# Optimization experiments

Hardware: AMD Instinct MI355X
Metric: run time of the kernel (lower is better)

The kernel has to match this reference:

```python
import jax, jax.numpy as jnp
import numpy as np

B, T, C, H, HS = 4, 2048, 1024, 16, 64
EPS = 1e-5


def setup_inputs() -> dict:
    key = jax.random.key(0)
    ks = jax.random.split(key, 16)
    s = lambda k, shp, fan: jax.random.normal(k, shp, jnp.float32) * (fan ** -0.5)
    return {
        "x": jax.random.normal(ks[0], (B, T, C), jnp.float32),
        "wq": s(ks[1], (H, C, HS), C), "bq": jnp.zeros((H, HS), jnp.float32),
        "wk": s(ks[2], (H, C, HS), C), "bk": jnp.zeros((H, HS), jnp.float32),
        "wv": s(ks[3], (H, C, HS), C), "bv": jnp.zeros((H, HS), jnp.float32),
        "wp": s(ks[4], (C, C), C), "bp": jnp.zeros((C,), jnp.float32),
        "w1": s(ks[5], (C, 4 * C), C), "b1": jnp.zeros((4 * C,), jnp.float32),
        "w2": s(ks[6], (4 * C, C), 4 * C), "b2": jnp.zeros((C,), jnp.float32),
        "g1": jnp.ones((C,), jnp.float32), "be1": jnp.zeros((C,), jnp.float32),
        "g2": jnp.ones((C,), jnp.float32), "be2": jnp.zeros((C,), jnp.float32),
    }


def _layernorm(x, g, b):
    mu = jnp.mean(x, axis=-1, keepdims=True)
    var = jnp.mean(jnp.square(x - mu), axis=-1, keepdims=True)
    return (x - mu) * jax.lax.rsqrt(var + EPS) * g + b


def reference(x, wq, bq, wk, bk, wv, bv, wp, bp, w1, b1, w2, b2, g1, be1, g2, be2):
    Bc, Tc, Cc = x.shape
    h = _layernorm(x, g1, be1)
    # per-head projections stacked: [B,H,T,HS]
    q = jnp.einsum('btc,hcd->bhtd', h, wq) + bq[None, :, None, :]
    k = jnp.einsum('btc,hcd->bhtd', h, wk) + bk[None, :, None, :]
    v = jnp.einsum('btc,hcd->bhtd', h, wv) + bv[None, :, None, :]
    # NOTE: source scales by 1/sqrt(n_embd), not 1/sqrt(head_size)
    scores = jnp.einsum('bhtd,bhsd->bhts', q, k) * (Cc ** -0.5)
    causal = jnp.tril(jnp.ones((Tc, Tc), bool))
    scores = jnp.where(causal, scores, -jnp.inf)
    attn = jax.nn.softmax(scores, axis=-1)
    out = jnp.einsum('bhts,bhsd->bhtd', attn, v)
    out = out.transpose(0, 2, 1, 3).reshape(Bc, Tc, Cc)  # concat heads
    x = x + out @ wp + bp
    h2 = _layernorm(x, g2, be2)
    ffn = jax.nn.relu(h2 @ w1 + b1) @ w2 + b2
    return x + ffn
```

## Files before the change

kernel.cpp:

```cpp
#include <hip/hip_runtime.h>


constexpr int Bb = 4, Tt = 2048, Cc = 1024, Hh = 16, HSz = 64, Ff = 4096;
constexpr int Mrows = Bb * Tt;

typedef __attribute__((ext_vector_type(8))) short bf16x8;
typedef __attribute__((ext_vector_type(4))) float f32x4;

__device__ __forceinline__ ushort f2bf(float f) {
  uint u = __builtin_bit_cast(uint, f);
  uint r = (u + 0x7fffu + ((u >> 16) & 1u)) >> 16;
  return (ushort)r;
}
__device__ __forceinline__ float bf2f(ushort s) {
  return __builtin_bit_cast(float, ((uint)s) << 16);
}
__device__ __forceinline__ uint cvtpk_bf16(float lo, float hi) {
  uint r;
  asm("v_cvt_pk_bf16_f32 %0, %1, %2" : "=v"(r) : "v"(lo), "v"(hi));
  return r;
}
__device__ __forceinline__ void gload16(const void* g, void* l) {
  __builtin_amdgcn_global_load_lds(
      (const __attribute__((address_space(1))) void*)g,
      (__attribute__((address_space(3))) void*)l, 16, 0, 0);
}
#define VMCNT(n) asm volatile("s_waitcnt vmcnt(" #n ")" ::: "memory")
#define LGKM0                                          \
  do {                                                 \
    asm volatile("s_waitcnt lgkmcnt(0)" ::: "memory"); \
    __builtin_amdgcn_sched_barrier(0);                 \
  } while (0)
#define BARRIER __builtin_amdgcn_s_barrier()

__device__ __forceinline__ void ln_body(const float* __restrict__ x,
                                        const float* __restrict__ g,
                                        const float* __restrict__ b,
                                        ushort* __restrict__ out, int row) {
  const float* xr = x + (size_t)row * Cc;
  int c4 = threadIdx.x * 4;
  float4 v = *(const float4*)(xr + c4);
  float s1 = v.x + v.y + v.z + v.w;
  float s2 = v.x * v.x + v.y * v.y + v.z * v.z + v.w * v.w;
#pragma unroll
  for (int off = 32; off >= 1; off >>= 1) {
    s1 += __shfl_xor(s1, off);
    s2 += __shfl_xor(s2, off);
  }
  __shared__ float red[8];
  int wid = threadIdx.x >> 6, lane = threadIdx.x & 63;
  if (lane == 0) { red[wid] = s1; red[4 + wid] = s2; }
  __syncthreads();
  float t1 = red[0] + red[1] + red[2] + red[3];
  float t2 = red[4] + red[5] + red[6] + red[7];
  float mu = t1 * (1.0f / Cc);
  float var = t2 * (1.0f / Cc) - mu * mu;
  float rs = rsqrtf(var + 1e-5f);
  float4 gv = *(const float4*)(g + c4);
  float4 bv = *(const float4*)(b + c4);
  ushort4 o;
  o.x = f2bf((v.x - mu) * rs * gv.x + bv.x);
  o.y = f2bf((v.y - mu) * rs * gv.y + bv.y);
  o.z = f2bf((v.z - mu) * rs * gv.z + bv.z);
  o.w = f2bf((v.w - mu) * rs * gv.w + bv.w);
  *(ushort4*)(out + (size_t)row * Cc + c4) = o;
}

__global__ __launch_bounds__(256) void ln_kernel(const float* __restrict__ x,
                                                 const float* __restrict__ g,
                                                 const float* __restrict__ b,
                                                 ushort* __restrict__ out) {
  ln_body(x, g, b, out, blockIdx.x);
}

__device__ __forceinline__ void tcast_body(const float* __restrict__ src,
                                           ushort* __restrict__ dst, int ldS,
                                           int ldD, int r0, int c0) {
  __shared__ float t[32][33];
  int c = threadIdx.x & 31, r8 = threadIdx.x >> 5;
#pragma unroll
  for (int i = 0; i < 4; ++i) {
    int r = r8 + i * 8;
    t[r][c] = src[(size_t)(r0 + r) * ldS + c0 + c];
  }
  __syncthreads();
#pragma unroll
  for (int i = 0; i < 4; ++i) {
    int rr = r8 + i * 8;
    dst[(size_t)(c0 + rr) * ldD + r0 + c] = f2bf(t[c][rr]);
  }
}

__global__ __launch_bounds__(256) void prep_kernel(
    const float* __restrict__ wq, const float* __restrict__ wk,
    const float* __restrict__ wv, const float* __restrict__ wp,
    const float* __restrict__ w1, const float* __restrict__ w2,
    const float* __restrict__ bq, const float* __restrict__ bk,
    const float* __restrict__ bv, ushort* __restrict__ wqkvT,
    ushort* __restrict__ wpT, ushort* __restrict__ w1T,
    ushort* __restrict__ w2T, float* __restrict__ bqkv,
    const float* __restrict__ x, const float* __restrict__ g1,
    const float* __restrict__ be1, ushort* __restrict__ h1b) {
  int id = blockIdx.x;
  if (id < 3072) {
    int z = id >> 6, rem = id & 63;
    int zz = z >> 4, h = z & 15;
    const float* src =
        (zz == 0 ? wq : (zz == 1 ? wk : wv)) + (size_t)h * Cc * HSz;
    ushort* d = wqkvT + (size_t)(zz * 1024 + h * 64) * 1024;
    tcast_body(src, d, HSz, Cc, (rem & 31) * 32, (rem >> 5) * 32);
  } else if (id < 4096) {
    int rem = id - 3072;
    tcast_body(wp, wpT, 1024, 1024, (rem & 31) * 32, (rem >> 5) * 32);
  } else if (id < 8192) {
    int rem = id - 4096;
    tcast_body(w1, w1T, 4096, 1024, (rem & 31) * 32, (rem >> 5) * 32);
  } else if (id < 12288) {
    int rem = id - 8192;
    tcast_body(w2, w2T, 1024, 4096, (rem & 127) * 32, (rem >> 7) * 32);
  } else if (id < 12300) {
    int i = (id - 12288) * 256 + threadIdx.x;
    bqkv[i] = i < 1024 ? bq[i] : (i < 2048 ? bk[i - 1024] : bv[i - 2048]);
  } else {
    ln_body(x, g1, be1, h1b, id - 12300);
  }
}

__device__ __forceinline__ void xcd_swz(int& bx, int& by) {
  int bid = blockIdx.x + blockIdx.y * gridDim.x;
  int cpx = (gridDim.x * gridDim.y) >> 3;
  int id = (bid & 7) * cpx + (bid >> 3);
  bx = id % gridDim.x;
  by = id / gridDim.x;
}

template <int MH, int NH>
__device__ __forceinline__ void mfma16(f32x4 (&acc)[8][4], bf16x8 (&a)[4][2],
                                       bf16x8 (&b)[2][2]) {
#pragma unroll
  for (int m = 0; m < 4; ++m)
#pragma unroll
    for (int n = 0; n < 2; ++n)
#pragma unroll
      for (int kk = 0; kk < 2; ++kk)
        acc[MH * 4 + m][NH * 2 + n] = __builtin_amdgcn_mfma_f32_16x16x32_bf16(
            a[m][kk], b[n][kk], acc[MH * 4 + m][NH * 2 + n], 0, 0, 0);
}

__device__ __forceinline__ void gemm256_main(const ushort* __restrict__ A,
                                             const ushort* __restrict__ Bt,
                                             int m0, int n0,
                                             ushort* __restrict__ As,
                                             ushort* __restrict__ Bs,
                                             f32x4 (&acc)[8][4]) {
  constexpr int NKT = 16;
  int tid = threadIdx.x, wid = tid >> 6, lane = tid & 63;
  int wr = wid >> 2, wc = wid & 3, fr = lane & 15, fq = lane >> 4;
  const ushort* Ag = A + (size_t)m0 * 1024;
  const ushort* Bg = Bt + (size_t)n0 * 1024;
  int r0 = tid >> 3, r1 = 64 + (tid >> 3);
  int sc = ((tid & 7) ^ ((tid >> 3) & 7)) << 3;

  auto stage = [&](int ktn, int h, int ns) {
    const ushort* g = (h < 2) ? Ag : Bg;
    ushort* l = ((h < 2) ? As : Bs) + ns * 16384 + (h & 1) * 8192;
    int kcol = ktn * 64, rbase = (h & 1) * 128;
    gload16(g + (size_t)(rbase + r0) * 1024 + kcol + sc, l + (size_t)wid * 512);
    gload16(g + (size_t)(rbase + r1) * 1024 + kcol + sc,
            l + (size_t)(512 + wid * 64) * 8);
  };
  auto readA = [&](int slot, int mh, bf16x8 (&a)[4][2]) {
#pragma unroll
    for (int m = 0; m < 4; ++m) {
      int row = wr * 128 + mh * 64 + m * 16 + fr;
#pragma unroll
      for (int kk = 0; kk < 2; ++kk)
        a[m][kk] = *(const bf16x8*)&As[slot * 16384 + row * 64 +
                                       (((kk * 4 + fq) ^ (row & 7)) << 3)];
    }
  };
  auto readB = [&](int slot, int nh, bf16x8 (&b)[2][2]) {
#pragma unroll
    for (int n = 0; n < 2; ++n) {
      int row = wc * 64 + nh * 32 + n * 16 + fr;
#pragma unroll
      for (int kk = 0; kk < 2; ++kk)
        b[n][kk] = *(const bf16x8*)&Bs[slot * 16384 + row * 64 +
                                       (((kk * 4 + fq) ^ (row & 7)) << 3)];
    }
  };

  stage(0, 0, 0); stage(0, 1, 0); stage(0, 2, 0); stage(0, 3, 0);
  VMCNT(0);
  BARRIER;

  bf16x8 a[4][2], b0[2][2], b1[2][2];
#pragma unroll 1
  for (int kt = 0; kt < NKT; ++kt) {
    int slot = kt & 1, ns = slot ^ 1;
    bool st = (kt + 1 < NKT);
    readA(slot, 0, a);
    readB(slot, 0, b0);
    if (st) { stage(kt + 1, 0, ns); stage(kt + 1, 2, ns); }
    BARRIER;
    LGKM0;
    __builtin_amdgcn_s_setprio(1);
    mfma16<0, 0>(acc, a, b0);
    __builtin_amdgcn_s_setprio(0);
    BARRIER;
    readB(slot, 1, b1);
    if (st) { stage(kt + 1, 1, ns); stage(kt + 1, 3, ns); }
    BARRIER;
    LGKM0;
    __builtin_amdgcn_s_setprio(1);
    mfma16<0, 1>(acc, a, b1);
    __builtin_amdgcn_s_setprio(0);
    BARRIER;
    readA(slot, 1, a);
    BARRIER;
    LGKM0;
    __builtin_amdgcn_s_setprio(1);
    mfma16<1, 0>(acc, a, b0);
    __builtin_amdgcn_s_setprio(0);
    BARRIER;
    __builtin_amdgcn_s_setprio(1);
    mfma16<1, 1>(acc, a, b1);
    __builtin_amdgcn_s_setprio(0);
    VMCNT(0);
    BARRIER;
  }
}

__global__ __launch_bounds__(512, 2) void gemm256_relu(
    const ushort* __restrict__ A, const ushort* __restrict__ Bt,
    const float* __restrict__ bias, ushort* __restrict__ Cout, int ldc) {
  __shared__ __align__(16) ushort As[2 * 256 * 64];
  __shared__ __align__(16) ushort Bs[2 * 256 * 64];
  f32x4 acc[8][4] = {};
  int bx, by;
  xcd_swz(bx, by);
  int m0 = by * 256, n0 = bx * 256;
  gemm256_main(A, Bt, m0, n0, As, Bs, acc);
  int lane = threadIdx.x & 63, wid = threadIdx.x >> 6;
  int wr = wid >> 2, wc = wid & 3, fr = lane & 15, fq = lane >> 4;
#pragma unroll
  for (int i = 0; i < 8; ++i) {
    int gm = m0 + wr * 128 + (i >> 2) * 64 + (i & 3) * 16 + fq * 4;
#pragma unroll
    for (int j2 = 0; j2 < 4; ++j2) {
      int gn = n0 + wc * 64 + (j2 >> 1) * 32 + (j2 & 1) * 16 + fr;
      float bsv = bias[gn];
#pragma unroll
      for (int j = 0; j < 4; ++j)
        Cout[(size_t)(gm + j) * ldc + gn] = f2bf(fmaxf(acc[i][j2][j] + bsv, 0.f));
    }
  }
}

__global__ __launch_bounds__(512, 2) void gemm192_qkv(
    const ushort* __restrict__ A, const ushort* __restrict__ Bt,
    const float* __restrict__ bias, ushort* __restrict__ q,
    ushort* __restrict__ k, ushort* __restrict__ vt) {
  __shared__ __align__(16) ushort As[2 * 256 * 64];
  __shared__ __align__(16) ushort Bs[2 * 192 * 64];
  f32x4 acc[8][3] = {};
  int bx, by;
  xcd_swz(bx, by);
  int m0 = by * 256, n0 = bx * 192;
  int tid = threadIdx.x, wid = tid >> 6, lane = tid & 63;
  int wr = wid >> 2, wc = wid & 3, fr = lane & 15, fq = lane >> 4;
  const ushort* Ag = A + (size_t)m0 * 1024;
  const ushort* Bg = Bt + (size_t)n0 * 1024;
  int r0 = tid >> 3;
  int sc = ((tid & 7) ^ ((tid >> 3) & 7)) << 3;
  constexpr int NKT = 16;

  auto stageA = [&](int ktn, int c, int ns) {
    ushort* l = As + ns * 16384 + c * 4096;
    gload16(Ag + (size_t)(c * 64 + r0) * 1024 + ktn * 64 + sc,
            l + (size_t)wid * 512);
  };
  auto stageB = [&](int ktn, int c, int ns) {
    ushort* l = Bs + ns * 12288 + c * 4096;
    gload16(Bg + (size_t)(c * 64 + r0) * 1024 + ktn * 64 + sc,
            l + (size_t)wid * 512);
  };
  auto readA = [&](int slot, int mh, bf16x8 (&a)[4][2]) {
#pragma unroll
    for (int m = 0; m < 4; ++m) {
      int row = wr * 128 + mh * 64 + m * 16 + fr;
#pragma unroll
      for (int kk = 0; kk < 2; ++kk)
        a[m][kk] = *(const bf16x8*)&As[slot * 16384 + row * 64 +
                                       (((kk * 4 + fq) ^ (row & 7)) << 3)];
    }
  };
  auto readB = [&](int slot, int nh, bf16x8 (&b)[2]) {
    int row = wc * 48 + nh * 16 + fr;
#pragma unroll
    for (int kk = 0; kk < 2; ++kk)
      b[kk] = *(const bf16x8*)&Bs[slot * 12288 + row * 64 +
                                  (((kk * 4 + fq) ^ (row & 7)) << 3)];
  };
  auto mfma16n = [&](int nh, bf16x8 (&a0)[4][2], bf16x8 (&a1)[4][2],
                     bf16x8 (&b)[2]) {
#pragma unroll
    for (int m = 0; m < 4; ++m)
#pragma unroll
      for (int kk = 0; kk < 2; ++kk)
        acc[m][nh] = __builtin_amdgcn_mfma_f32_16x16x32_bf16(
            a0[m][kk], b[kk], acc[m][nh], 0, 0, 0);
#pragma unroll
    for (int m = 0; m < 4; ++m)
#pragma unroll
      for (int kk = 0; kk < 2; ++kk)
        acc[4 + m][nh] = __builtin_amdgcn_mfma_f32_16x16x32_bf16(
            a1[m][kk], b[kk], acc[4 + m][nh], 0, 0, 0);
  };

  stageA(0, 0, 0); stageA(0, 1, 0); stageA(0, 2, 0); stageA(0, 3, 0);
  stageB(0, 0, 0); stageB(0, 1, 0); stageB(0, 2, 0);
  VMCNT(0);
  BARRIER;

  bf16x8 a0[4][2], a1[4][2], b0[2], b1[2], b2[2];
#pragma unroll 1
  for (int kt = 0; kt < NKT; ++kt) {
    int slot = kt & 1, ns = slot ^ 1;
    bool st = (kt + 1 < NKT);
    readA(slot, 0, a0);
    readA(slot, 1, a1);
    readB(slot, 0, b0);
    if (st) { stageA(kt + 1, 0, ns); stageA(kt + 1, 1, ns); stageB(kt + 1, 0, ns); }
    BARRIER;
    LGKM0;
    __builtin_amdgcn_s_setprio(1);
    mfma16n(0, a0, a1, b0);
    __builtin_amdgcn_s_setprio(0);
    BARRIER;
    readB(slot, 1, b1);
    if (st) { stageA(kt + 1, 2, ns); stageA(kt + 1, 3, ns); stageB(kt + 1, 1, ns); }
    BARRIER;
    LGKM0;
    __builtin_amdgcn_s_setprio(1);
    mfma16n(1, a0, a1, b1);
    __builtin_amdgcn_s_setprio(0);
    BARRIER;
    readB(slot, 2, b2);
    if (st) { stageB(kt + 1, 2, ns); }
    BARRIER;
    LGKM0;
    __builtin_amdgcn_s_setprio(1);
    mfma16n(2, a0, a1, b2);
    __builtin_amdgcn_s_setprio(0);
    VMCNT(0);
    BARRIER;
  }

  const float qscale = 1.4426950408889634f / 32.0f;
#pragma unroll
  for (int i = 0; i < 8; ++i) {
    int gm = m0 + wr * 128 + (i >> 2) * 64 + (i & 3) * 16 + fq * 4;
#pragma unroll
    for (int nh = 0; nh < 3; ++nh) {
      int gn = n0 + wc * 48 + nh * 16 + fr;
      float bsv = bias[gn];
      if (gn < 1024) {
#pragma unroll
        for (int j = 0; j < 4; ++j)
          q[(size_t)(gm + j) * 1024 + gn] = f2bf((acc[i][nh][j] + bsv) * qscale);
      } else if (gn < 2048) {
        int col = gn - 1024;
#pragma unroll
        for (int j = 0; j < 4; ++j)
          k[(size_t)(gm + j) * 1024 + col] = f2bf(acc[i][nh][j] + bsv);
      } else {
        int dd = gn - 2048, h = dd >> 6, d = dd & 63;
        int bbr = gm >> 11, t = gm & 2047;
        ushort4 pw = {f2bf(acc[i][nh][0] + bsv), f2bf(acc[i][nh][1] + bsv),
                      f2bf(acc[i][nh][2] + bsv), f2bf(acc[i][nh][3] + bsv)};
        *(ushort4*)&vt[(((size_t)(bbr * 16 + h)) * 64 + d) * 2048 + t] = pw;
      }
    }
  }
}

__device__ __forceinline__ void gemm_main(const ushort* __restrict__ A, int lda,
                                          const ushort* __restrict__ Bt, int ldb,
                                          int K, int m0, int n0,
                                          ushort* __restrict__ As,
                                          ushort* __restrict__ Bs,
                                          f32x4 (&acc)[4][2]) {
  int tid = threadIdx.x, wid = tid >> 6, lane = tid & 63;
  int wr = wid >> 2, wc = wid & 3, fr = lane & 15, fq = lane >> 4;
  const ushort* Ag = A + (size_t)m0 * lda;
  const ushort* Bg = Bt + (size_t)n0 * ldb;
  int NKT = K >> 6;
  auto stage = [&](int ktn, int sl) {
#pragma unroll
    for (int c = 0; c < 2; ++c) {
      int slot = c * 512 + tid;
      int row = slot >> 3, s = slot & 7;
      int sw = (s << 3) ^ ((row & 7) << 3);
      gload16(Ag + (size_t)row * lda + ktn * 64 + sw,
              As + sl * 8192 + (size_t)(c * 512 + wid * 64) * 8);
      gload16(Bg + (size_t)row * ldb + ktn * 64 + sw,
              Bs + sl * 8192 + (size_t)(c * 512 + wid * 64) * 8);
    }
  };

  stage(0, 0);
#pragma unroll 1
  for (int kt = 0; kt < NKT; ++kt) {
    int c = kt & 1;
    __syncthreads();
    if (kt + 1 < NKT) stage(kt + 1, c ^ 1);
    bf16x8 av[4][2], bv[2][2];
#pragma unroll
    for (int m = 0; m < 4; ++m) {
      int row = wr * 64 + m * 16 + fr;
#pragma unroll
      for (int ks = 0; ks < 2; ++ks)
        av[m][ks] = *(const bf16x8*)&As[c * 8192 + row * 64 +
                                        (((ks * 4 + fq) ^ (row & 7)) << 3)];
    }
#pragma unroll
    for (int n = 0; n < 2; ++n) {
      int row = wc * 32 + n * 16 + fr;
#pragma unroll
      for (int ks = 0; ks < 2; ++ks)
        bv[n][ks] = *(const bf16x8*)&Bs[c * 8192 + row * 64 +
                                        (((ks * 4 + fq) ^ (row & 7)) << 3)];
    }
    __builtin_amdgcn_s_setprio(1);
#pragma unroll
    for (int m = 0; m < 4; ++m)
#pragma unroll
      for (int n = 0; n < 2; ++n)
#pragma unroll
        for (int ks = 0; ks < 2; ++ks)
          acc[m][n] = __builtin_amdgcn_mfma_f32_16x16x32_bf16(
              av[m][ks], bv[n][ks], acc[m][n], 0, 0, 0);
    __builtin_amdgcn_s_setprio(0);
  }
}

template <bool RELU, bool HASRES, bool OUTBF16>
__global__ __launch_bounds__(512) void gemm_bf16(
    const ushort* __restrict__ A, int lda, const ushort* __restrict__ Bt,
    int ldb, const float* __restrict__ bias, const float* __restrict__ res,
    void* __restrict__ Cout, int ldc, int K) {
  __shared__ __align__(16) ushort As[2 * 128 * 64];
  __shared__ __align__(16) ushort Bs[2 * 128 * 64];
  f32x4 acc[4][2] = {};
  int bx, by;
  xcd_swz(bx, by);
  int m0 = by * 128, n0 = bx * 128;
  gemm_main(A, lda, Bt, ldb, K, m0, n0, As, Bs, acc);
  int lane = threadIdx.x & 63, wid = threadIdx.x >> 6;
  int wr = wid >> 2, wc = wid & 3, fr = lane & 15, fq = lane >> 4;
#pragma unroll
  for (int m = 0; m < 4; ++m) {
    int gm = m0 + wr * 64 + m * 16 + fq * 4;
#pragma unroll
    for (int n = 0; n < 2; ++n) {
      int gn = n0 + wc * 32 + n * 16 + fr;
      float bsv = bias[gn];
#pragma unroll
      for (int j = 0; j < 4; ++j) {
        int row = gm + j;
        float v = acc[m][n][j] + bsv;
        if constexpr (HASRES) v += res[(size_t)row * ldc + gn];
        if constexpr (RELU) v = fmaxf(v, 0.f);
        if constexpr (OUTBF16)
          ((ushort*)Cout)[(size_t)row * ldc + gn] = f2bf(v);
        else
          ((float*)Cout)[(size_t)row * ldc + gn] = v;
      }
    }
  }
}

constexpr int QB = 128, KVB = 64;
__global__ __launch_bounds__(512) void attn_kernel(const ushort* __restrict__ Qb,
                                                   const ushort* __restrict__ Kb,
                                                   const ushort* __restrict__ Vt,
                                                   ushort* __restrict__ att) {
  __shared__ __align__(16) ushort Klds[2][64 * 64];
  __shared__ __align__(16) ushort Vlds[2][64 * 64];
  __shared__ __align__(16) ushort Plds[8][16 * 64];
  int tid = threadIdx.x, wid = tid >> 6, lane = tid & 63;
  int fr = lane & 15, fq = lane >> 4;
  int bh = blockIdx.y, bb = bh >> 4, hh = bh & 15;
  const ushort* qkbase = Qb + ((size_t)bb * Tt) * Cc + hh * HSz;
  const ushort* Kbase = Kb + ((size_t)bb * Tt) * Cc + hh * HSz;
  const ushort* Vbase = Vt + ((size_t)(bb * Hh + hh)) * HSz * Tt;
  int srow = tid >> 3;
  int ssw = ((tid & 7) << 3) ^ ((srow & 7) << 3);
  bf16x8 vones;
#pragma unroll
  for (int i = 0; i < 8; ++i) vones[i] = (short)0x3F80;

#pragma unroll 1
  for (int pass = 0; pass < 2; ++pass) {
    int qt = pass ? (Tt / QB - 1 - (int)blockIdx.x) : (int)blockIdx.x;
    int q0 = qt * QB;
    int q0w = q0 + wid * 16;

    bf16x8 Qreg[2];
#pragma unroll
    for (int d2 = 0; d2 < 2; ++d2)
      Qreg[d2] = *(const bf16x8*)(qkbase + (size_t)(q0w + fr) * Cc + d2 * 32 + fq * 8);
    f32x4 Oa[4] = {};
    f32x4 Ol = {};
    float mrow = -1e30f;
    int nt = q0 / KVB + 2;

    __syncthreads();
    gload16(Kbase + (size_t)srow * Cc + ssw, (char*)Klds[0] + wid * 1024);
    gload16(Vbase + (size_t)srow * Tt + ssw, (char*)Vlds[0] + wid * 1024);

#pragma unroll 1
    for (int kt = 0; kt < nt; ++kt) {
      int t0 = kt * KVB;
      int c = kt & 1;
      __syncthreads();
      if (kt + 1 < nt) {
        int t0n = t0 + KVB;
        gload16(Kbase + (size_t)(t0n + srow) * Cc + ssw,
                (char*)Klds[c ^ 1] + wid * 1024);
        gload16(Vbase + (size_t)srow * Tt + t0n + ssw,
                (char*)Vlds[c ^ 1] + wid * 1024);
      }
      if (q0w + 15 < t0) continue;

      const char* Kc = (const char*)Klds[c];
      const char* Vc = (const char*)Vlds[c];
      bf16x8 kf[4][2];
#pragma unroll
      for (int ks = 0; ks < 4; ++ks)
#pragma unroll
        for (int d2 = 0; d2 < 2; ++d2) {
          int row = ks * 16 + fr;
          int off = (d2 * 64 + fq * 16) ^ ((row & 7) << 4);
          kf[ks][d2] = *(const bf16x8*)(Kc + row * 128 + off);
        }
      f32x4 accs[4] = {};
      __builtin_amdgcn_s_setprio(1);
#pragma unroll
      for (int ks = 0; ks < 4; ++ks) {
        accs[ks] = __builtin_amdgcn_mfma_f32_16x16x32_bf16(
            kf[ks][0], Qreg[0], accs[ks], 0, 0, 0);
        accs[ks] = __builtin_amdgcn_mfma_f32_16x16x32_bf16(
            kf[ks][1], Qreg[1], accs[ks], 0, 0, 0);
      }
      __builtin_amdgcn_s_setprio(0);

      float sv[4][4];
      if (t0 + 63 <= q0w) {
#pragma unroll
        for (int ks = 0; ks < 4; ++ks)
#pragma unroll
          for (int j = 0; j < 4; ++j) sv[ks][j] = accs[ks][j];
      } else {
        int qg = q0w + fr;
#pragma unroll
        for (int ks = 0; ks < 4; ++ks)
#pragma unroll
          for (int j = 0; j < 4; ++j) {
            int kg = t0 + ks * 16 + fq * 4 + j;
            sv[ks][j] = (kg <= qg) ? accs[ks][j] : -1e30f;
          }
      }
      float m0a = fmaxf(fmaxf(sv[0][0], sv[0][1]), fmaxf(sv[0][2], sv[0][3]));
      float m1a = fmaxf(fmaxf(sv[1][0], sv[1][1]), fmaxf(sv[1][2], sv[1][3]));
      float m2a = fmaxf(fmaxf(sv[2][0], sv[2][1]), fmaxf(sv[2][2], sv[2][3]));
      float m3a = fmaxf(fmaxf(sv[3][0], sv[3][1]), fmaxf(sv[3][2], sv[3][3]));
      float vmax = fmaxf(fmaxf(m0a, m1a), fmaxf(m2a, m3a));

      float mnew = mrow;
      if (!__all(vmax <= mrow + 11.0f)) {
        float rmax = fmaxf(vmax, __shfl_xor(vmax, 16));
        rmax = fmaxf(rmax, __shfl_xor(rmax, 32));
        mnew = fmaxf(mrow, rmax);
        float sf = exp2f(mrow - mnew);
        mrow = mnew;
#pragma unroll
        for (int j = 0; j < 4; ++j) {
          float sfo = __shfl(sf, fq * 4 + j);
          Ol[j] *= sfo;
#pragma unroll
          for (int ds = 0; ds < 4; ++ds) Oa[ds][j] *= sfo;
        }
      }
      char* pbase = (char*)Plds[wid] + fr * 128;
#pragma unroll
      for (int ks = 0; ks < 4; ++ks) {
        float p0 = exp2f(sv[ks][0] - mnew);
        float p1 = exp2f(sv[ks][1] - mnew);
        float p2 = exp2f(sv[ks][2] - mnew);
        float p3 = exp2f(sv[ks][3] - mnew);
        uint2 pw = {cvtpk_bf16(p0, p1), cvtpk_bf16(p2, p3)};
        int off = (ks * 32 + fq * 8) ^ ((fr & 7) << 4);
        *(uint2*)(pbase + off) = pw;
      }

      bf16x8 vf[4][2];
#pragma unroll
      for (int ds = 0; ds < 4; ++ds)
#pragma unroll
        for (int k2 = 0; k2 < 2; ++k2) {
          int row = ds * 16 + fr;
          int off = (k2 * 64 + fq * 16) ^ ((row & 7) << 4);
          vf[ds][k2] = *(const bf16x8*)(Vc + row * 128 + off);
        }
      bf16x8 pf[2];
#pragma unroll
      for (int k2 = 0; k2 < 2; ++k2) {
        int off = (k2 * 64 + fq * 16) ^ ((fr & 7) << 4);
        pf[k2] = *(const bf16x8*)((const char*)Plds[wid] + fr * 128 + off);
      }
      __builtin_amdgcn_s_setprio(1);
#pragma unroll
      for (int ds = 0; ds < 4; ++ds) {
        Oa[ds] = __builtin_amdgcn_mfma_f32_16x16x32_bf16(
            pf[0], vf[ds][0], Oa[ds], 0, 0, 0);
        Oa[ds] = __builtin_amdgcn_mfma_f32_16x16x32_bf16(
            pf[1], vf[ds][1], Oa[ds], 0, 0, 0);
      }
      Ol = __builtin_amdgcn_mfma_f32_16x16x32_bf16(pf[0], vones, Ol, 0, 0, 0);
      Ol = __builtin_amdgcn_mfma_f32_16x16x32_bf16(pf[1], vones, Ol, 0, 0, 0);
      __builtin_amdgcn_s_setprio(0);
    }

#pragma unroll
    for (int j = 0; j < 4; ++j) {
      float lo = 1.f / Ol[j];
      int qg = q0w + fq * 4 + j;
      ushort* orow = att + (size_t)(bb * Tt + qg) * Cc + hh * HSz;
#pragma unroll
      for (int ds = 0; ds < 4; ++ds)
        orow[ds * 16 + fr] = f2bf(Oa[ds][j] * lo);
    }
  }
}

extern "C" void kernel_launch(void* const* d_in, const int* in_sizes, int n_in,
                              void* d_out, int out_size, void* d_ws,
                              size_t ws_size, hipStream_t stream) {
  const float* x = (const float*)d_in[0];
  const float* wq = (const float*)d_in[1];
  const float* bq = (const float*)d_in[2];
  const float* wk = (const float*)d_in[3];
  const float* bk = (const float*)d_in[4];
  const float* wv = (const float*)d_in[5];
  const float* bv = (const float*)d_in[6];
  const float* wp = (const float*)d_in[7];
  const float* bp = (const float*)d_in[8];
  const float* w1 = (const float*)d_in[9];
  const float* b1 = (const float*)d_in[10];
  const float* w2 = (const float*)d_in[11];
  const float* b2 = (const float*)d_in[12];
  const float* g1 = (const float*)d_in[13];
  const float* be1 = (const float*)d_in[14];
  const float* g2 = (const float*)d_in[15];
  const float* be2 = (const float*)d_in[16];
  float* out = (float*)d_out;

  ushort* Qb = (ushort*)d_ws;
  ushort* Kb = Qb + (size_t)8388608;
  ushort* Vt = Kb + (size_t)8388608;
  ushort* att = Vt + (size_t)8388608;
  ushort* ffh = Qb;
  ushort* h1b = att + (size_t)8388608;
  float* x2 = (float*)(h1b + (size_t)8388608);
  ushort* wqkvT = (ushort*)(x2 + (size_t)8388608);
  ushort* wpT = wqkvT + (size_t)3145728;
  ushort* w1T = wpT + (size_t)1048576;
  ushort* w2T = w1T + (size_t)4194304;
  float* bqkv = (float*)(w2T + (size_t)4194304);

  prep_kernel<<<dim3(20492), 256, 0, stream>>>(wq, wk, wv, wp, w1, w2, bq, bk,
                                               bv, wqkvT, wpT, w1T, w2T, bqkv,
                                               x, g1, be1, h1b);
  gemm192_qkv<<<dim3(16, 32), 512, 0, stream>>>(h1b, wqkvT, bqkv, Qb, Kb, Vt);
  attn_kernel<<<dim3(Tt / QB / 2, Bb * Hh), 512, 0, stream>>>(Qb, Kb, Vt, att);
  gemm_bf16<false, true, false><<<dim3(8, 64), 512, 0, stream>>>(
      att, 1024, wpT, 1024, bp, x, x2, 1024, 1024);
  ln_kernel<<<dim3(Mrows), 256, 0, stream>>>(x2, g2, be2, h1b);
  gemm256_relu<<<dim3(16, 32), 512, 0, stream>>>(h1b, w1T, b1, ffh, 4096);
  gemm_bf16<false, true, false><<<dim3(8, 64), 512, 0, stream>>>(
      ffh, 4096, w2T, 4096, b2, x2, out, 1024, 4096);
}
```

Measured before the change: 338.2 us.

## Share K/V tiles between paired causal query tiles in one attention pass

The attention kernel used to handle its two query tiles (early and mirrored late) in two sequential passes, each streaming K/V from global memory. Now both tiles are processed in a single KV loop: each loaded K/V tile is applied to the late tile and, while still causally needed, the early tile. This removes the duplicate K/V loads and barriers of the first pass. The cost is doubled per-thread accumulator state (two Q fragments, O, l and m sets) with added launch bounds asking for 4 blocks, which could cause register pressure or spills.

```diff
diff --git a/kernel.cpp b/kernel.cpp
--- a/kernel.cpp
+++ b/kernel.cpp
@@ -482,10 +482,9 @@
 }
 
 constexpr int QB = 128, KVB = 64;
-__global__ __launch_bounds__(512) void attn_kernel(const ushort* __restrict__ Qb,
-                                                   const ushort* __restrict__ Kb,
-                                                   const ushort* __restrict__ Vt,
-                                                   ushort* __restrict__ att) {
+__global__ __launch_bounds__(512, 4) void attn_kernel(
+    const ushort* __restrict__ Qb, const ushort* __restrict__ Kb,
+    const ushort* __restrict__ Vt, ushort* __restrict__ att) {
   __shared__ __align__(16) ushort Klds[2][64 * 64];
   __shared__ __align__(16) ushort Vlds[2][64 * 64];
   __shared__ __align__(16) ushort Plds[8][16 * 64];
@@ -501,146 +500,146 @@
 #pragma unroll
   for (int i = 0; i < 8; ++i) vones[i] = (short)0x3F80;
 
+  int qtA = blockIdx.x, qtB = (Tt / QB - 1) - blockIdx.x;
+  int q0wA = qtA * QB + wid * 16, q0wB = qtB * QB + wid * 16;
+  int NT = qtB * 2 + 2;
+
+  bf16x8 QregA[2], QregB[2];
+#pragma unroll
+  for (int d2 = 0; d2 < 2; ++d2) {
+    QregA[d2] = *(const bf16x8*)(qkbase + (size_t)(q0wA + fr) * Cc + d2 * 32 + fq * 8);
+    QregB[d2] = *(const bf16x8*)(qkbase + (size_t)(q0wB + fr) * Cc + d2 * 32 + fq * 8);
+  }
+  f32x4 OaA[4] = {}, OaB[4] = {};
+  f32x4 OlA = {}, OlB = {};
+  float mrowA = -1e30f, mrowB = -1e30f;
+
+  char* pbase = (char*)Plds[wid] + fr * 128;
+
+  auto process = [&](int q0w, bf16x8 (&Qreg)[2], f32x4 (&Oa)[4], f32x4& Ol,
+                     float& mrow, int t0, const char* Kc, const char* Vc) {
+    bf16x8 kf[4][2];
+#pragma unroll
+    for (int ks = 0; ks < 4; ++ks)
+#pragma unroll
+      for (int d2 = 0; d2 < 2; ++d2) {
+        int row = ks * 16 + fr;
+        int off = (d2 * 64 + fq * 16) ^ ((row & 7) << 4);
+        kf[ks][d2] = *(const bf16x8*)(Kc + row * 128 + off);
+      }
+    f32x4 accs[4] = {};
+    __builtin_amdgcn_s_setprio(1);
+#pragma unroll
+    for (int ks = 0; ks < 4; ++ks) {
+      accs[ks] = __builtin_amdgcn_mfma_f32_16x16x32_bf16(
+          kf[ks][0], Qreg[0], accs[ks], 0, 0, 0);
+      accs[ks] = __builtin_amdgcn_mfma_f32_16x16x32_bf16(
+          kf[ks][1], Qreg[1], accs[ks], 0, 0, 0);
+    }
+    __builtin_amdgcn_s_setprio(0);
+
+    float sv[4][4];
+    if (t0 + 63 <= q0w) {
+#pragma unroll
+      for (int ks = 0; ks < 4; ++ks)
+#pragma unroll
+        for (int j = 0; j < 4; ++j) sv[ks][j] = accs[ks][j];
+    } else {
+      int qg = q0w + fr;
+#pragma unroll
+      for (int ks = 0; ks < 4; ++ks)
+#pragma unroll
+        for (int j = 0; j < 4; ++j) {
+          int kg = t0 + ks * 16 + fq * 4 + j;
+          sv[ks][j] = (kg <= qg) ? accs[ks][j] : -1e30f;
+        }
+    }
+    float m0a = fmaxf(fmaxf(sv[0][0], sv[0][1]), fmaxf(sv[0][2], sv[0][3]));
+    float m1a = fmaxf(fmaxf(sv[1][0], sv[1][1]), fmaxf(sv[1][2], sv[1][3]));
+    float m2a = fmaxf(fmaxf(sv[2][0], sv[2][1]), fmaxf(sv[2][2], sv[2][3]));
+    float m3a = fmaxf(fmaxf(sv[3][0], sv[3][1]), fmaxf(sv[3][2], sv[3][3]));
+    float vmax = fmaxf(fmaxf(m0a, m1a), fmaxf(m2a, m3a));
+
+    float mnew = mrow;
+    if (!__all(vmax <= mrow + 11.0f)) {
+      float rmax = fmaxf(vmax, __shfl_xor(vmax, 16));
+      rmax = fmaxf(rmax, __shfl_xor(rmax, 32));
+      mnew = fmaxf(mrow, rmax);
+      float sf = exp2f(mrow - mnew);
+      mrow = mnew;
+#pragma unroll
+      for (int j = 0; j < 4; ++j) {
+        float sfo = __shfl(sf, fq * 4 + j);
+        Ol[j] *= sfo;
+#pragma unroll
+        for (int ds = 0; ds < 4; ++ds) Oa[ds][j] *= sfo;
+      }
+    }
+#pragma unroll
+    for (int ks = 0; ks < 4; ++ks) {
+      float p0 = exp2f(sv[ks][0] - mnew);
+      float p1 = exp2f(sv[ks][1] - mnew);
+      float p2 = exp2f(sv[ks][2] - mnew);
+      float p3 = exp2f(sv[ks][3] - mnew);
+      uint2 pw = {cvtpk_bf16(p0, p1), cvtpk_bf16(p2, p3)};
+      int off = (ks * 32 + fq * 8) ^ ((fr & 7) << 4);
+      *(uint2*)(pbase + off) = pw;
+    }
+
+    bf16x8 pf[2];
+#pragma unroll
+    for (int k2 = 0; k2 < 2; ++k2) {
+      int off = (k2 * 64 + fq * 16) ^ ((fr & 7) << 4);
+      pf[k2] = *(const bf16x8*)((const char*)Plds[wid] + fr * 128 + off);
+    }
+    __builtin_amdgcn_s_setprio(1);
+#pragma unroll
+    for (int ds = 0; ds < 4; ++ds) {
+      bf16x8 vf0, vf1;
+      int row = ds * 16 + fr;
+      vf0 = *(const bf16x8*)(Vc + row * 128 + ((0 * 64 + fq * 16) ^ ((row & 7) << 4)));
+      vf1 = *(const bf16x8*)(Vc + row * 128 + ((1 * 64 + fq * 16) ^ ((row & 7) << 4)));
+      Oa[ds] = __builtin_amdgcn_mfma_f32_16x16x32_bf16(pf[0], vf0, Oa[ds], 0, 0, 0);
+      Oa[ds] = __builtin_amdgcn_mfma_f32_16x16x32_bf16(pf[1], vf1, Oa[ds], 0, 0, 0);
+    }
+    Ol = __builtin_amdgcn_mfma_f32_16x16x32_bf16(pf[0], vones, Ol, 0, 0, 0);
+    Ol = __builtin_amdgcn_mfma_f32_16x16x32_bf16(pf[1], vones, Ol, 0, 0, 0);
+    __builtin_amdgcn_s_setprio(0);
+  };
+
+  gload16(Kbase + (size_t)srow * Cc + ssw, (char*)Klds[0] + wid * 1024);
+  gload16(Vbase + (size_t)srow * Tt + ssw, (char*)Vlds[0] + wid * 1024);
+
 #pragma unroll 1
-  for (int pass = 0; pass < 2; ++pass) {
-    int qt = pass ? (Tt / QB - 1 - (int)blockIdx.x) : (int)blockIdx.x;
-    int q0 = qt * QB;
-    int q0w = q0 + wid * 16;
-
-    bf16x8 Qreg[2];
-#pragma unroll
-    for (int d2 = 0; d2 < 2; ++d2)
-      Qreg[d2] = *(const bf16x8*)(qkbase + (size_t)(q0w + fr) * Cc + d2 * 32 + fq * 8);
-    f32x4 Oa[4] = {};
-    f32x4 Ol = {};
-    float mrow = -1e30f;
-    int nt = q0 / KVB + 2;
-
+  for (int kt = 0; kt < NT; ++kt) {
+    int t0 = kt * KVB;
+    int c = kt & 1;
     __syncthreads();
-    gload16(Kbase + (size_t)srow * Cc + ssw, (char*)Klds[0] + wid * 1024);
-    gload16(Vbase + (size_t)srow * Tt + ssw, (char*)Vlds[0] + wid * 1024);
-
-#pragma unroll 1
-    for (int kt = 0; kt < nt; ++kt) {
-      int t0 = kt * KVB;
-      int c = kt & 1;
-      __syncthreads();
-      if (kt + 1 < nt) {
-        int t0n = t0 + KVB;
-        gload16(Kbase + (size_t)(t0n + srow) * Cc + ssw,
-                (char*)Klds[c ^ 1] + wid * 1024);
-        gload16(Vbase + (size_t)srow * Tt + t0n + ssw,
-                (char*)Vlds[c ^ 1] + wid * 1024);
-      }
-      if (q0w + 15 < t0) continue;
-
-      const char* Kc = (const char*)Klds[c];
-      const char* Vc = (const char*)Vlds[c];
-      bf16x8 kf[4][2];
-#pragma unroll
-      for (int ks = 0; ks < 4; ++ks)
-#pragma unroll
-        for (int d2 = 0; d2 < 2; ++d2) {
-          int row = ks * 16 + fr;
-          int off = (d2 * 64 + fq * 16) ^ ((row & 7) << 4);
-          kf[ks][d2] = *(const bf16x8*)(Kc + row * 128 + off);
-        }
-      f32x4 accs[4] = {};
-      __builtin_amdgcn_s_setprio(1);
-#pragma unroll
-      for (int ks = 0; ks < 4; ++ks) {
-        accs[ks] = __builtin_amdgcn_mfma_f32_16x16x32_bf16(
-            kf[ks][0], Qreg[0], accs[ks], 0, 0, 0);
-        accs[ks] = __builtin_amdgcn_mfma_f32_16x16x32_bf16(
-            kf[ks][1], Qreg[1], accs[ks], 0, 0, 0);
-      }
-      __builtin_amdgcn_s_setprio(0);
-
-      float sv[4][4];
-      if (t0 + 63 <= q0w) {
-#pragma unroll
-        for (int ks = 0; ks < 4; ++ks)
-#pragma unroll
-          for (int j = 0; j < 4; ++j) sv[ks][j] = accs[ks][j];
-      } else {
-        int qg = q0w + fr;
-#pragma unroll
-        for (int ks = 0; ks < 4; ++ks)
-#pragma unroll
-          for (int j = 0; j < 4; ++j) {
-            int kg = t0 + ks * 16 + fq * 4 + j;
-            sv[ks][j] = (kg <= qg) ? accs[ks][j] : -1e30f;
-          }
-      }
-      float m0a = fmaxf(fmaxf(sv[0][0], sv[0][1]), fmaxf(sv[0][2], sv[0][3]));
-      float m1a = fmaxf(fmaxf(sv[1][0], sv[1][1]), fmaxf(sv[1][2], sv[1][3]));
-      float m2a = fmaxf(fmaxf(sv[2][0], sv[2][1]), fmaxf(sv[2][2], sv[2][3]));
-      float m3a = fmaxf(fmaxf(sv[3][0], sv[3][1]), fmaxf(sv[3][2], sv[3][3]));
-      float vmax = fmaxf(fmaxf(m0a, m1a), fmaxf(m2a, m3a));
-
-      float mnew = mrow;
-      if (!__all(vmax <= mrow + 11.0f)) {
-        float rmax = fmaxf(vmax, __shfl_xor(vmax, 16));
-        rmax = fmaxf(rmax, __shfl_xor(rmax, 32));
-        mnew = fmaxf(mrow, rmax);
-        float sf = exp2f(mrow - mnew);
-        mrow = mnew;
-#pragma unroll
-        for (int j = 0; j < 4; ++j) {
-          float sfo = __shfl(sf, fq * 4 + j);
-          Ol[j] *= sfo;
-#pragma unroll
-          for (int ds = 0; ds < 4; ++ds) Oa[ds][j] *= sfo;
-        }
-      }
-      char* pbase = (char*)Plds[wid] + fr * 128;
-#pragma unroll
-      for (int ks = 0; ks < 4; ++ks) {
-        float p0 = exp2f(sv[ks][0] - mnew);
-        float p1 = exp2f(sv[ks][1] - mnew);
-        float p2 = exp2f(sv[ks][2] - mnew);
-        float p3 = exp2f(sv[ks][3] - mnew);
-        uint2 pw = {cvtpk_bf16(p0, p1), cvtpk_bf16(p2, p3)};
-        int off = (ks * 32 + fq * 8) ^ ((fr & 7) << 4);
-        *(uint2*)(pbase + off) = pw;
-      }
-
-      bf16x8 vf[4][2];
-#pragma unroll
-      for (int ds = 0; ds < 4; ++ds)
-#pragma unroll
-        for (int k2 = 0; k2 < 2; ++k2) {
-          int row = ds * 16 + fr;
-          int off = (k2 * 64 + fq * 16) ^ ((row & 7) << 4);
-          vf[ds][k2] = *(const bf16x8*)(Vc + row * 128 + off);
-        }
-      bf16x8 pf[2];
-#pragma unroll
-      for (int k2 = 0; k2 < 2; ++k2) {
-        int off = (k2 * 64 + fq * 16) ^ ((fr & 7) << 4);
-        pf[k2] = *(const bf16x8*)((const char*)Plds[wid] + fr * 128 + off);
-      }
-      __builtin_amdgcn_s_setprio(1);
-#pragma unroll
-      for (int ds = 0; ds < 4; ++ds) {
-        Oa[ds] = __builtin_amdgcn_mfma_f32_16x16x32_bf16(
-            pf[0], vf[ds][0], Oa[ds], 0, 0, 0);
-        Oa[ds] = __builtin_amdgcn_mfma_f32_16x16x32_bf16(
-            pf[1], vf[ds][1], Oa[ds], 0, 0, 0);
-      }
-      Ol = __builtin_amdgcn_mfma_f32_16x16x32_bf16(pf[0], vones, Ol, 0, 0, 0);
-      Ol = __builtin_amdgcn_mfma_f32_16x16x32_bf16(pf[1], vones, Ol, 0, 0, 0);
-      __builtin_amdgcn_s_setprio(0);
-    }
-
-#pragma unroll
-    for (int j = 0; j < 4; ++j) {
-      float lo = 1.f / Ol[j];
-      int qg = q0w + fq * 4 + j;
-      ushort* orow = att + (size_t)(bb * Tt + qg) * Cc + hh * HSz;
-#pragma unroll
-      for (int ds = 0; ds < 4; ++ds)
-        orow[ds * 16 + fr] = f2bf(Oa[ds][j] * lo);
+    if (kt + 1 < NT) {
+      int t0n = t0 + KVB;
+      gload16(Kbase + (size_t)(t0n + srow) * Cc + ssw,
+              (char*)Klds[c ^ 1] + wid * 1024);
+      gload16(Vbase + (size_t)srow * Tt + t0n + ssw,
+              (char*)Vlds[c ^ 1] + wid * 1024);
+    }
+    const char* Kc = (const char*)Klds[c];
+    const char* Vc = (const char*)Vlds[c];
+    if (!(q0wB + 15 < t0)) process(q0wB, QregB, OaB, OlB, mrowB, t0, Kc, Vc);
+    if (!(q0wA + 15 < t0)) process(q0wA, QregA, OaA, OlA, mrowA, t0, Kc, Vc);
+  }
+
+#pragma unroll
+  for (int j = 0; j < 4; ++j) {
+    float loA = 1.f / OlA[j];
+    float loB = 1.f / OlB[j];
+    int qgA = q0wA + fq * 4 + j;
+    int qgB = q0wB + fq * 4 + j;
+    ushort* orowA = att + (size_t)(bb * Tt + qgA) * Cc + hh * HSz;
+    ushort* orowB = att + (size_t)(bb * Tt + qgB) * Cc + hh * HSz;
+#pragma unroll
+    for (int ds = 0; ds < 4; ++ds) {
+      orowA[ds * 16 + fr] = f2bf(OaA[ds][j] * loA);
+      orowB[ds * 16 + fr] = f2bf(OaB[ds][j] * loB);
     }
   }
 }
```

Measured after the change: 340.8 us. Within noise of the previous version (+0.7%).
